# Performance work log

Hardware: AMD Instinct MI355X
Metric: run time of the kernel (lower is better)

The kernel has to match this reference:

```python
import jax, jax.numpy as jnp
import numpy as np

MAX_SHIFT = 20
DAILY_CYCLE = 288
HORIZON_OFFSET = 1


def _valid_shifts(T):
    shifts = sorted(set(list(range(-MAX_SHIFT, 1)) + [-(DAILY_CYCLE - HORIZON_OFFSET)]))
    return [s for s in shifts if 0 < abs(s) < T]


def setup_inputs() -> dict:
    key = jax.random.key(0)
    k1, k2 = jax.random.split(key)
    x = jax.random.normal(k1, (2, 320, 207, 64), dtype=jnp.float32)
    w = jax.random.normal(k2, (1, 1), dtype=jnp.float32)  # LearnableSimilarity linear weight
    return {"x": x, "w": w}


def reference(x, w):
    B, T, L, D = x.shape
    shifts = _valid_shifts(T)
    S = len(shifts)  # 21 for T=320

    # Build zero-padded shifted copies: for s<0, shifted[:, t] = x[:, t+|s|] (zeros at tail).
    sh_list = []
    for s in shifts:
        p = abs(s)
        pad = jnp.zeros((B, p, L, D), dtype=x.dtype)
        if s < 0:
            sh_list.append(jnp.concatenate([x[:, p:], pad], axis=1))
        else:
            sh_list.append(jnp.concatenate([pad, x[:, :-p]], axis=1))
    xs = jnp.stack(sh_list, axis=1)  # [B, S, T, L, D]

    # Learnable similarity = (x . y) * w; mean over T fused into the einsum.
    wscalar = w[0, 0]
    sim_avg = jnp.einsum('btld,bstmd->bslm', x, xs) * (wscalar / T)  # [B,S,L,L]  l=target, m=shifted

    # Faithful to original: softmax over joint (S*target-L) axis, then raw reshape to (L, S*L).
    flat = sim_avg.reshape(B, S * L, L)
    soft = jax.nn.softmax(flat, axis=1)
    attn = soft.reshape(B, L, S * L)  # NOTE: reshape, not transpose (matches torch .view)

    x_flat = xs.transpose(0, 2, 1, 3, 4).reshape(B, T, S * L, D)  # m index = s*L + link
    out = jnp.einsum('btmd,blm->btld', x_flat, attn)  # [B,T,L,D]
    return out
```

## Files before the change

kernel.cpp:

```cpp
#include <hip/hip_runtime.h>
#include <hip/hip_bf16.h>

#define B_DIM 2
#define T_DIM 320
#define L_DIM 207
#define D_DIM 64
#define S_DIM 21
#define J_TOT (S_DIM * L_DIM)
#define MPAD 224
#define IPAD 256
#define NSPLIT 4
#define TSPLIT 80
#define NCH_A 32
#define CH_A 136
#define NCH_P 128
#define CH_P 34
#define LD_ROW (L_DIM * D_DIM)
#define SLAB_B 26496

typedef __attribute__((ext_vector_type(8))) short bf16x8;
typedef __attribute__((ext_vector_type(4))) float f32x4;

__device__ inline unsigned short f2bf(float f) {
    unsigned int u = __builtin_bit_cast(unsigned int, f);
    u = (u + 0x7FFFu + ((u >> 16) & 1u)) >> 16;
    return (unsigned short)u;
}

__device__ inline int shift_p(int s) { return (s == 0) ? 287 : (21 - s); }
__device__ inline int imin(int a, int b) { return a < b ? a : b; }
__device__ inline int imax(int a, int b) { return a > b ? a : b; }

__device__ __forceinline__ void glds16(const void* g, void* l) {
    __builtin_amdgcn_global_load_lds(
        (const __attribute__((address_space(1))) void*)g,
        (__attribute__((address_space(3))) void*)l,
        16, 0, 0);
}

__global__ void __launch_bounds__(256) k_prep(const float* __restrict__ x,
                                              unsigned short* __restrict__ xbf,
                                              unsigned short* __restrict__ xt) {
    __shared__ float tile[L_DIM * 66];
    int bt = blockIdx.x;
    const float* src = x + (size_t)bt * LD_ROW;
    int tid = threadIdx.x;
    for (int idx = tid; idx < L_DIM * D_DIM; idx += 256) {
        int l = idx >> 6, d = idx & 63;
        tile[l * 66 + d] = src[idx];
    }
    __syncthreads();
    unsigned short* dst1 = xbf + (size_t)bt * LD_ROW;
    for (int idx = tid; idx < L_DIM * D_DIM; idx += 256) {
        int l = idx >> 6, d = idx & 63;
        dst1[idx] = f2bf(tile[l * 66 + d]);
    }
    unsigned short* dst2 = xt + (size_t)bt * (7 * 64 * 32);
    if (tid < MPAD) {
        int mc = tid >> 5, mi = tid & 31;
        for (int d = 0; d < D_DIM; ++d) {
            float v = (tid < L_DIM) ? tile[tid * 66 + d] : 0.0f;
            dst2[(mc * 64 + d) * 32 + mi] = f2bf(v);
        }
    }
}

__global__ void __launch_bounds__(512, 2) k_simr(const unsigned short* __restrict__ xbf,
                                                 const unsigned short* __restrict__ zpage,
                                                 float* __restrict__ part) {
    __shared__ __align__(16) unsigned short Asl[4][2048];
    __shared__ __align__(16) unsigned short Bsl[24][2048];

    int id = blockIdx.x;
    int split = id / 98;
    int r2 = id % 98;
    int b = r2 & 1;
    int pb = r2 >> 1;
    int lfb = pb / 7, mfb = pb % 7;

    int t0 = split * TSPLIT;
    int t1 = t0 + TSPLIT;

    int tid = threadIdx.x;
    int w = tid >> 6, lane = tid & 63;
    int wl = w & 1, wm = (w >> 1) & 1, h = w >> 2;
    int fr = lane & 15, kg = lane >> 4;
    int x7 = fr & 7;

    int lf = lfb * 2 + wl;
    int mf = mfb * 2 + wm;
    bool wvalid = (lf <= 12) && (mf <= 12);

    bool isA = (w < 4);
    int gq = (w & 3) * 64 + lane;
    int grow = gq >> 3, gc = gq & 7;
    int srcoff = grow * 128 + ((gc ^ (grow & 7)) * 16);
    int dstoff = (w & 3) * 1024;

    const char* xb = (const char*)xbf;
    size_t abase = (size_t)b * T_DIM * SLAB_B + lfb * 4096;
    size_t bbase = (size_t)b * T_DIM * SLAB_B + mfb * 4096;

    int lrA = wl * 16 + fr, lrB = wm * 16 + fr;
    int c0 = ((0 + kg) ^ x7) * 16, c1 = ((4 + kg) ^ x7) * 16;
    int aoff0 = lrA * 128 + c0, aoff1 = lrA * 128 + c1;
    int boff0 = lrB * 128 + c0, boff1 = lrB * 128 + c1;

    f32x4 acc[10];
#pragma unroll
    for (int j = 0; j < 10; ++j) acc[j] = f32x4{0.f, 0.f, 0.f, 0.f};
    bf16x8 ring[10][2];

    if (isA) {
        glds16(xb + abase + (size_t)t0 * SLAB_B + srcoff, (char*)Asl[t0 & 3] + dstoff);
    } else {
        for (int k = 1; k <= 20; ++k) {
            int tau = t0 + k;
            const char* src = (tau < T_DIM) ? (xb + bbase + (size_t)tau * SLAB_B) : (const char*)zpage;
            glds16(src + srcoff, (char*)Bsl[tau % 24] + dstoff);
        }
    }
    asm volatile("s_waitcnt vmcnt(0)" ::: "memory");
    __builtin_amdgcn_s_barrier();
    asm volatile("" ::: "memory");
    if (wvalid) {
#pragma unroll
        for (int j = 1; j <= 9; ++j) {
            int tau = t0 + 20 - 10 * h - j;
            const char* sb = (const char*)Bsl[tau % 24];
            ring[10 - j][0] = *(const bf16x8*)(sb + boff0);
            ring[10 - j][1] = *(const bf16x8*)(sb + boff1);
        }
    }

    for (int tb = t0; tb < t1; tb += 10) {
#pragma unroll
        for (int u = 0; u < 10; ++u) {
            int t = tb + u;
            if (isA) {
                int tn = t + 1;
                const char* src = (tn < T_DIM) ? (xb + abase + (size_t)tn * SLAB_B) : (const char*)zpage;
                glds16(src + srcoff, (char*)Asl[tn & 3] + dstoff);
            } else {
                int tau = t + 21;
                const char* src = (tau < T_DIM) ? (xb + bbase + (size_t)tau * SLAB_B) : (const char*)zpage;
                glds16(src + srcoff, (char*)Bsl[tau % 24] + dstoff);
            }
            asm volatile("s_waitcnt vmcnt(1)" ::: "memory");
            __builtin_amdgcn_s_barrier();
            asm volatile("" ::: "memory");
            if (wvalid) {
                const char* sa = (const char*)Asl[t & 3];
                bf16x8 a0 = *(const bf16x8*)(sa + aoff0);
                bf16x8 a1 = *(const bf16x8*)(sa + aoff1);
                int tauf = t + 20 - 10 * h;
                const char* sb = (const char*)Bsl[tauf % 24];
                ring[u][0] = *(const bf16x8*)(sb + boff0);
                ring[u][1] = *(const bf16x8*)(sb + boff1);
#pragma unroll
                for (int j = 0; j < 10; ++j) {
                    acc[j] = __builtin_amdgcn_mfma_f32_16x16x32_bf16(a0, ring[(u - j + 10) % 10][0], acc[j], 0, 0, 0);
                    acc[j] = __builtin_amdgcn_mfma_f32_16x16x32_bf16(a1, ring[(u - j + 10) % 10][1], acc[j], 0, 0, 0);
                }
            }
        }
    }

    int col = mf * 16 + fr;
    if (col < L_DIM) {
        float* pbase = part + (size_t)(split * B_DIM + b) * J_TOT * L_DIM;
#pragma unroll
        for (int j = 0; j < 10; ++j) {
            int s = 10 * h + 1 + j;
#pragma unroll
            for (int r = 0; r < 4; ++r) {
                int row = lf * 16 + kg * 4 + r;
                if (row < L_DIM)
                    pbase[((size_t)s * L_DIM + row) * L_DIM + col] = acc[j][r];
            }
        }
    }
}

__global__ void __launch_bounds__(256) k_sim0(const unsigned short* __restrict__ xbf,
                                              float* __restrict__ part) {
    __shared__ __align__(16) unsigned short S[2][2][8192];

    int id = blockIdx.x;
    int tile = id & 3;
    int rest = id >> 2;
    int split = rest & 3;
    int b = rest >> 2;
    int l0 = (tile >> 1) * 128, m0 = (tile & 1) * 128;

    const int p = 287;
    int nt = T_DIM - p;
    int t0 = (split * nt) >> 2;
    int t1 = (((split + 1) * nt) >> 2);

    int tid = threadIdx.x;
    int wave = tid >> 6, lane = tid & 63;
    int wl = wave >> 1, wm = wave & 1;
    int fr = lane & 15, kg = lane >> 4;
    int x7 = fr & 7;

    int rN = 0, cN = 0;
#pragma unroll
    for (int g = 0; g < 4; ++g) {
        if (l0 + (g * 2 + wl) * 16 < L_DIM) rN = g + 1;
        if (m0 + (g * 2 + wm) * 16 < L_DIM) cN = g + 1;
    }

    int srcoff[4];
#pragma unroll
    for (int i = 0; i < 4; ++i) {
        int n = i * 256 + wave * 64 + lane;
        int row = n >> 3, c = n & 7;
        srcoff[i] = row * 128 + ((c ^ (row & 7)) * 16);
    }
    int wbase = wave * 1024;

    int cb0 = (kg ^ x7) * 16, cb1 = ((4 + kg) ^ x7) * 16;
    int aro[4], bro[4];
#pragma unroll
    for (int g = 0; g < 4; ++g) {
        aro[g] = ((g * 2 + wl) * 16 + fr) * 128;
        bro[g] = ((g * 2 + wm) * 16 + fr) * 128;
    }

    f32x4 acc[4][4];
#pragma unroll
    for (int i = 0; i < 4; ++i)
#pragma unroll
        for (int j = 0; j < 4; ++j) acc[i][j] = f32x4{0.f, 0.f, 0.f, 0.f};

    const size_t LDB = (size_t)LD_ROW * 2;
    const char* abase = (const char*)xbf + ((size_t)b * T_DIM * LD_ROW + (size_t)l0 * 64) * 2;
    const char* bbase = (const char*)xbf + ((size_t)(b * T_DIM + p) * LD_ROW + (size_t)m0 * 64) * 2;

    if (t1 > t0) {
        {
            const char* a = abase + (size_t)t0 * LDB;
            const char* bb = bbase + (size_t)t0 * LDB;
            char* lA = (char*)&S[0][0][0] + wbase;
            char* lB = (char*)&S[0][1][0] + wbase;
#pragma unroll
            for (int i = 0; i < 4; ++i) {
                glds16(a + srcoff[i], lA + i * 4096);
                glds16(bb + srcoff[i], lB + i * 4096);
            }
        }
        int cur = 0;
        for (int t = t0; t < t1; ++t) {
            bool more = (t + 1 < t1);
            if (more) {
                const char* a = abase + (size_t)(t + 1) * LDB;
                const char* bb = bbase + (size_t)(t + 1) * LDB;
                char* lA = (char*)&S[cur ^ 1][0][0] + wbase;
                char* lB = (char*)&S[cur ^ 1][1][0] + wbase;
#pragma unroll
                for (int i = 0; i < 4; ++i) {
                    glds16(a + srcoff[i], lA + i * 4096);
                    glds16(bb + srcoff[i], lB + i * 4096);
                }
                asm volatile("s_waitcnt vmcnt(8)" ::: "memory");
            } else {
                asm volatile("s_waitcnt vmcnt(0)" ::: "memory");
            }
            __builtin_amdgcn_s_barrier();
            asm volatile("" ::: "memory");
            const char* lA = (const char*)&S[cur][0][0];
            const char* lB = (const char*)&S[cur][1][0];
#pragma unroll
            for (int kd = 0; kd < 2; ++kd) {
                int cb = kd ? cb1 : cb0;
                bf16x8 af[4], bv[4];
#pragma unroll
                for (int g = 0; g < 4; ++g)
                    if (g < rN) af[g] = *(const bf16x8*)(lA + aro[g] + cb);
#pragma unroll
                for (int g = 0; g < 4; ++g)
                    if (g < cN) bv[g] = *(const bf16x8*)(lB + bro[g] + cb);
#pragma unroll
                for (int rg = 0; rg < 4; ++rg)
                    if (rg < rN)
#pragma unroll
                        for (int cg = 0; cg < 4; ++cg)
                            if (cg < cN)
                                acc[rg][cg] = __builtin_amdgcn_mfma_f32_16x16x32_bf16(
                                    af[rg], bv[cg], acc[rg][cg], 0, 0, 0);
            }
            asm volatile("" ::: "memory");
            __builtin_amdgcn_s_barrier();
            cur ^= 1;
        }
    }

    float* pdst = part + ((size_t)(split * B_DIM + b) * J_TOT + (size_t)0 * L_DIM) * L_DIM;
#pragma unroll
    for (int rg = 0; rg < 4; ++rg)
#pragma unroll
        for (int cg = 0; cg < 4; ++cg) {
            int col = m0 + (cg * 2 + wm) * 16 + fr;
            if (col < L_DIM) {
#pragma unroll
                for (int r = 0; r < 4; ++r) {
                    int row = l0 + (rg * 2 + wl) * 16 + kg * 4 + r;
                    if (row < L_DIM) pdst[(size_t)row * L_DIM + col] = acc[rg][cg][r];
                }
            }
        }
}

__global__ void __launch_bounds__(256) k_sumexp(const float* __restrict__ part,
                                                const float* __restrict__ w,
                                                float* __restrict__ psum) {
    int c = blockIdx.x, b = blockIdx.y;
    int m = threadIdx.x;
    if (m >= L_DIM) return;
    float scale = w[0] / (float)T_DIM;
    int j0 = c * CH_A, j1 = imin(j0 + CH_A, J_TOT);
    float acc = 0.0f;
    for (int j = j0; j < j1; ++j) {
        float v = 0.0f;
#pragma unroll
        for (int r = 0; r < NSPLIT; ++r)
            v += part[((size_t)(r * B_DIM + b) * J_TOT + j) * L_DIM + m];
        acc += __expf(v * scale);
    }
    psum[(b * NCH_A + c) * L_DIM + m] = acc;
}

__global__ void __launch_bounds__(256) k_pack(const float* __restrict__ part,
                                              const float* __restrict__ w,
                                              const float* __restrict__ psum,
                                              unsigned short* __restrict__ pp) {
    __shared__ float sinv[L_DIM];
    int c = blockIdx.x, b = blockIdx.y;
    int tid = threadIdx.x;
    if (tid < L_DIM) {
        float g = 0.0f;
        for (int q = 0; q < NCH_A; ++q) g += psum[(b * NCH_A + q) * L_DIM + tid];
        sinv[tid] = 1.0f / g;
    }
    __syncthreads();
    if (tid >= MPAD) return;
    float scale = w[0] / (float)T_DIM;
    float inv = (tid < L_DIM) ? sinv[tid] : 0.0f;
    int mc = tid >> 5, mi = tid & 31;
    int j0 = c * CH_P, j1 = imin(j0 + CH_P, J_TOT);
    for (int j = j0; j < j1; ++j) {
        float pr = 0.0f;
        if (tid < L_DIM) {
            float v = 0.0f;
#pragma unroll
            for (int r = 0; r < NSPLIT; ++r)
                v += part[((size_t)(r * B_DIM + b) * J_TOT + j) * L_DIM + tid];
            pr = __expf(v * scale) * inv;
        }
        int i = j / S_DIM, s = j % S_DIM;
        pp[((((size_t)b * S_DIM + s) * 7 + mc) * IPAD + i) * 32 + mi] = f2bf(pr);
    }
}

__global__ void __launch_bounds__(256) k_out(const unsigned short* __restrict__ ppn,
                                             const unsigned short* __restrict__ xtn,
                                             float* __restrict__ out) {
    __shared__ __align__(16) unsigned short As[2][128 * 32];
    __shared__ __align__(16) unsigned short Bs[2][2][64 * 32];

    int id = blockIdx.x;
    int low = id & 7;
    int b = low >> 2, tr = low & 3;
    int rest = id >> 3;
    int tg = rest >> 1;
    int ih = rest & 1;
    int t0 = tr * TSPLIT + tg * 2;
    int i0 = ih * 128;

    int tid = threadIdx.x;
    int wave = tid >> 6, lane = tid & 63;
    int wt = wave >> 1, wi = wave & 1;
    int fr = lane & 15, kg = lane >> 4;
    int t = t0 + wt;

    const char* ppb = (const char*)ppn + (size_t)b * (S_DIM * 7 * IPAD * 32) * 2;
    const char* xtb = (const char*)xtn + (size_t)b * (T_DIM * 7 * 64 * 32) * 2;

    int asrc[2], bsrc[2];
#pragma unroll
    for (int i = 0; i < 2; ++i) {
        int n = wave * 128 + i * 64 + lane;
        int row = n >> 2, c = n & 3;
        asrc[i] = row * 64 + ((c ^ ((row >> 1) & 3)) * 16);
        int n2 = (wave & 1) * 128 + i * 64 + lane;
        int row2 = n2 >> 2, c2 = n2 & 3;
        bsrc[i] = row2 * 64 + ((c2 ^ ((row2 >> 1) & 3)) * 16);
    }
    int btau = wave >> 1;

    int cb = (kg ^ ((fr >> 1) & 3)) * 16;
    int aro[4], bro[4];
#pragma unroll
    for (int g = 0; g < 4; ++g) {
        aro[g] = (wi * 64 + g * 16 + fr) * 64;
        bro[g] = (g * 16 + fr) * 64;
    }

    f32x4 acc[4][4];
#pragma unroll
    for (int i = 0; i < 4; ++i)
#pragma unroll
        for (int j = 0; j < 4; ++j) acc[i][j] = f32x4{0.f, 0.f, 0.f, 0.f};

    int has0 = (t0 <= 32) ? 1 : 0;
    int sBegin = imax(1, t0 - 298);
    int ns = (21 - sBegin) + has0;

    auto sOf = [&](int k) { return (has0 && k == 0) ? 0 : sBegin + (k - has0); };

    auto stage = [&](int ss, int mc, int buf) {
        const char* ga = ppb + (((size_t)(ss * 7 + mc) * IPAD + i0) * 32) * 2;
        char* lA = (char*)&As[buf][0] + wave * 2048;
        glds16(ga + asrc[0], lA);
        glds16(ga + asrc[1], lA + 1024);
        int pp_ = shift_p(ss);
        int tau = imin(t0 + btau + pp_, T_DIM - 1);
        const char* gb = xtb + ((size_t)tau * 7 + mc) * 4096;
        char* lB = (char*)&Bs[buf][btau][0] + (wave & 1) * 2048;
        glds16(gb + bsrc[0], lB);
        glds16(gb + bsrc[1], lB + 1024);
    };

    stage(sOf(0), 0, 0);
    int cur = 0;
    for (int k = 0; k < ns; ++k) {
        int s = sOf(k);
        int p = shift_p(s);
        bool valid = (t + p < T_DIM);
        for (int mc = 0; mc < 7; ++mc) {
            bool more = (mc < 6) || (k + 1 < ns);
            if (more) {
                int s2 = (mc < 6) ? s : sOf(k + 1);
                int mc2 = (mc < 6) ? mc + 1 : 0;
                stage(s2, mc2, cur ^ 1);
                asm volatile("s_waitcnt vmcnt(4)" ::: "memory");
            } else {
                asm volatile("s_waitcnt vmcnt(0)" ::: "memory");
            }
            __builtin_amdgcn_s_barrier();
            asm volatile("" ::: "memory");
            if (valid) {
                const char* lA = (const char*)&As[cur][0];
                const char* lB = (const char*)&Bs[cur][wt][0];
                bf16x8 af[4], bv[4];
#pragma unroll
                for (int g = 0; g < 4; ++g) af[g] = *(const bf16x8*)(lA + aro[g] + cb);
#pragma unroll
                for (int g = 0; g < 4; ++g) bv[g] = *(const bf16x8*)(lB + bro[g] + cb);
#pragma unroll
                for (int rg = 0; rg < 4; ++rg)
#pragma unroll
                    for (int cg = 0; cg < 4; ++cg)
                        acc[rg][cg] = __builtin_amdgcn_mfma_f32_16x16x32_bf16(
                            af[rg], bv[cg], acc[rg][cg], 0, 0, 0);
            }
            asm volatile("" ::: "memory");
            __builtin_amdgcn_s_barrier();
            cur ^= 1;
        }
    }

    float* obase = out + (size_t)(b * T_DIM + t) * LD_ROW;
#pragma unroll
    for (int rg = 0; rg < 4; ++rg)
#pragma unroll
        for (int cg = 0; cg < 4; ++cg) {
            int d = cg * 16 + fr;
#pragma unroll
            for (int r = 0; r < 4; ++r) {
                int i = i0 + wi * 64 + rg * 16 + kg * 4 + r;
                if (i < L_DIM) obase[(size_t)i * D_DIM + d] = acc[rg][cg][r];
            }
        }
}

extern "C" void kernel_launch(void* const* d_in, const int* in_sizes, int n_in,
                              void* d_out, int out_size, void* d_ws, size_t ws_size,
                              hipStream_t stream) {
    const float* x = (const float*)d_in[0];
    const float* w = (const float*)d_in[1];
    float* out = (float*)d_out;

    char* ws = (char*)d_ws;
    size_t off = 0;
    auto carve = [&](size_t bytes) {
        void* p = ws + off;
        off += (bytes + 255) & ~(size_t)255;
        return p;
    };
    unsigned short* xbf = (unsigned short*)carve((size_t)B_DIM * T_DIM * LD_ROW * 2);
    unsigned short* xt  = (unsigned short*)carve((size_t)B_DIM * T_DIM * 7 * 64 * 32 * 2);
    float* part         = (float*)carve((size_t)NSPLIT * B_DIM * J_TOT * L_DIM * 4);
    float* psum         = (float*)carve((size_t)B_DIM * NCH_A * L_DIM * 4);
    size_t pp_bytes = (size_t)B_DIM * S_DIM * 7 * IPAD * 32 * 2;
    unsigned short* pp  = (unsigned short*)carve(pp_bytes);
    unsigned short* zpage = (unsigned short*)carve(4096);

    k_prep<<<B_DIM * T_DIM, 256, 0, stream>>>(x, xbf, xt);
    hipMemsetAsync(zpage, 0, 4096, stream);
    k_simr<<<NSPLIT * 98, 512, 0, stream>>>(xbf, zpage, part);
    k_sim0<<<B_DIM * NSPLIT * 4, 256, 0, stream>>>(xbf, part);
    k_sumexp<<<dim3(NCH_A, B_DIM), 256, 0, stream>>>(part, w, psum);
    hipMemsetAsync(pp, 0, pp_bytes, stream);
    k_pack<<<dim3(NCH_P, B_DIM), 256, 0, stream>>>(part, w, psum, pp);
    k_out<<<640, 256, 0, stream>>>(pp, xt, out);
}
```

Measured before the change: 349.0 us.

## Deepen async prefetch pipelines in similarity and output GEMM kernels

The similarity kernel now prefetches A tiles three steps ahead in an 8-slot LDS ring and B tiles two more steps ahead, waiting on vmcnt(3) instead of vmcnt(1). The output kernel flattens its shift/chunk loops into one linear stage index with a 4-buffer ring, prefetches two stages ahead, and drops the trailing barrier per iteration. A softmax-related chunking constant also changes (NCH_A/CH_A). The aim is to hide global-load latency behind MFMA work. In exchange it uses more LDS, which may cut occupancy, and removing the second barrier relies on the 4-deep ring to keep buffers from being overwritten while still being read.

```diff
diff --git a/kernel.cpp b/kernel.cpp
--- a/kernel.cpp
+++ b/kernel.cpp
@@ -11,8 +11,8 @@
 #define IPAD 256
 #define NSPLIT 4
 #define TSPLIT 80
-#define NCH_A 32
-#define CH_A 136
+#define NCH_A 128
+#define CH_A 34
 #define NCH_P 128
 #define CH_P 34
 #define LD_ROW (L_DIM * D_DIM)
@@ -68,7 +68,7 @@
 __global__ void __launch_bounds__(512, 2) k_simr(const unsigned short* __restrict__ xbf,
                                                  const unsigned short* __restrict__ zpage,
                                                  float* __restrict__ part) {
-    __shared__ __align__(16) unsigned short Asl[4][2048];
+    __shared__ __align__(16) unsigned short Asl[8][2048];
     __shared__ __align__(16) unsigned short Bsl[24][2048];
 
     int id = blockIdx.x;
@@ -112,9 +112,12 @@
     bf16x8 ring[10][2];
 
     if (isA) {
-        glds16(xb + abase + (size_t)t0 * SLAB_B + srcoff, (char*)Asl[t0 & 3] + dstoff);
+#pragma unroll
+        for (int i = 0; i < 3; ++i)
+            glds16(xb + abase + (size_t)(t0 + i) * SLAB_B + srcoff,
+                   (char*)Asl[(t0 + i) & 7] + dstoff);
     } else {
-        for (int k = 1; k <= 20; ++k) {
+        for (int k = 1; k <= 22; ++k) {
             int tau = t0 + k;
             const char* src = (tau < T_DIM) ? (xb + bbase + (size_t)tau * SLAB_B) : (const char*)zpage;
             glds16(src + srcoff, (char*)Bsl[tau % 24] + dstoff);
@@ -138,19 +141,19 @@
         for (int u = 0; u < 10; ++u) {
             int t = tb + u;
             if (isA) {
-                int tn = t + 1;
+                int tn = t + 3;
                 const char* src = (tn < T_DIM) ? (xb + abase + (size_t)tn * SLAB_B) : (const char*)zpage;
-                glds16(src + srcoff, (char*)Asl[tn & 3] + dstoff);
+                glds16(src + srcoff, (char*)Asl[tn & 7] + dstoff);
             } else {
-                int tau = t + 21;
+                int tau = t + 23;
                 const char* src = (tau < T_DIM) ? (xb + bbase + (size_t)tau * SLAB_B) : (const char*)zpage;
                 glds16(src + srcoff, (char*)Bsl[tau % 24] + dstoff);
             }
-            asm volatile("s_waitcnt vmcnt(1)" ::: "memory");
+            asm volatile("s_waitcnt vmcnt(3)" ::: "memory");
             __builtin_amdgcn_s_barrier();
             asm volatile("" ::: "memory");
             if (wvalid) {
-                const char* sa = (const char*)Asl[t & 3];
+                const char* sa = (const char*)Asl[t & 7];
                 bf16x8 a0 = *(const bf16x8*)(sa + aoff0);
                 bf16x8 a1 = *(const bf16x8*)(sa + aoff1);
                 int tauf = t + 20 - 10 * h;
@@ -366,8 +369,8 @@
 __global__ void __launch_bounds__(256) k_out(const unsigned short* __restrict__ ppn,
                                              const unsigned short* __restrict__ xtn,
                                              float* __restrict__ out) {
-    __shared__ __align__(16) unsigned short As[2][128 * 32];
-    __shared__ __align__(16) unsigned short Bs[2][2][64 * 32];
+    __shared__ __align__(16) unsigned short As[4][128 * 32];
+    __shared__ __align__(16) unsigned short Bs[4][2][64 * 32];
 
     int id = blockIdx.x;
     int low = id & 7;
@@ -416,10 +419,12 @@
     int has0 = (t0 <= 32) ? 1 : 0;
     int sBegin = imax(1, t0 - 298);
     int ns = (21 - sBegin) + has0;
+    int Q = ns * 7;
 
     auto sOf = [&](int k) { return (has0 && k == 0) ? 0 : sBegin + (k - has0); };
 
-    auto stage = [&](int ss, int mc, int buf) {
+    auto stage = [&](int q, int buf) {
+        int ss = sOf(q / 7), mc = q % 7;
         const char* ga = ppb + (((size_t)(ss * 7 + mc) * IPAD + i0) * 32) * 2;
         char* lA = (char*)&As[buf][0] + wave * 2048;
         glds16(ga + asrc[0], lA);
@@ -432,43 +437,37 @@
         glds16(gb + bsrc[1], lB + 1024);
     };
 
-    stage(sOf(0), 0, 0);
-    int cur = 0;
-    for (int k = 0; k < ns; ++k) {
-        int s = sOf(k);
-        int p = shift_p(s);
-        bool valid = (t + p < T_DIM);
-        for (int mc = 0; mc < 7; ++mc) {
-            bool more = (mc < 6) || (k + 1 < ns);
-            if (more) {
-                int s2 = (mc < 6) ? s : sOf(k + 1);
-                int mc2 = (mc < 6) ? mc + 1 : 0;
-                stage(s2, mc2, cur ^ 1);
-                asm volatile("s_waitcnt vmcnt(4)" ::: "memory");
-            } else {
-                asm volatile("s_waitcnt vmcnt(0)" ::: "memory");
-            }
-            __builtin_amdgcn_s_barrier();
-            asm volatile("" ::: "memory");
-            if (valid) {
-                const char* lA = (const char*)&As[cur][0];
-                const char* lB = (const char*)&Bs[cur][wt][0];
-                bf16x8 af[4], bv[4];
-#pragma unroll
-                for (int g = 0; g < 4; ++g) af[g] = *(const bf16x8*)(lA + aro[g] + cb);
-#pragma unroll
-                for (int g = 0; g < 4; ++g) bv[g] = *(const bf16x8*)(lB + bro[g] + cb);
-#pragma unroll
-                for (int rg = 0; rg < 4; ++rg)
-#pragma unroll
-                    for (int cg = 0; cg < 4; ++cg)
-                        acc[rg][cg] = __builtin_amdgcn_mfma_f32_16x16x32_bf16(
-                            af[rg], bv[cg], acc[rg][cg], 0, 0, 0);
-            }
-            asm volatile("" ::: "memory");
-            __builtin_amdgcn_s_barrier();
-            cur ^= 1;
-        }
+    stage(0, 0);
+    stage(1, 1);
+    for (int q = 0; q < Q; ++q) {
+        if (q + 2 < Q) {
+            stage(q + 2, (q + 2) & 3);
+            asm volatile("s_waitcnt vmcnt(8)" ::: "memory");
+        } else if (q + 1 < Q) {
+            asm volatile("s_waitcnt vmcnt(4)" ::: "memory");
+        } else {
+            asm volatile("s_waitcnt vmcnt(0)" ::: "memory");
+        }
+        __builtin_amdgcn_s_barrier();
+        asm volatile("" ::: "memory");
+        int sc = sOf(q / 7);
+        int p = shift_p(sc);
+        if (t + p < T_DIM) {
+            const char* lA = (const char*)&As[q & 3][0];
+            const char* lB = (const char*)&Bs[q & 3][wt][0];
+            bf16x8 af[4], bv[4];
+#pragma unroll
+            for (int g = 0; g < 4; ++g) af[g] = *(const bf16x8*)(lA + aro[g] + cb);
+#pragma unroll
+            for (int g = 0; g < 4; ++g) bv[g] = *(const bf16x8*)(lB + bro[g] + cb);
+#pragma unroll
+            for (int rg = 0; rg < 4; ++rg)
+#pragma unroll
+                for (int cg = 0; cg < 4; ++cg)
+                    acc[rg][cg] = __builtin_amdgcn_mfma_f32_16x16x32_bf16(
+                        af[rg], bv[cg], acc[rg][cg], 0, 0, 0);
+        }
+        asm volatile("" ::: "memory");
     }
 
     float* obase = out + (size_t)(b * T_DIM + t) * LD_ROW;
```

After: 399.4 us. 14.4% more time.
